# Kernel optimization log

Hardware: AMD Instinct MI355X
Metric: run time of the kernel (lower is better)

Reference implementation:

```python
import jax, jax.numpy as jnp
import numpy as np

B, L, D = 32, 1024, 1024
H = 8            # hard-coded in FourierBlock weights1 leading dim
E = D // H       # 128
M = 64           # number of retained low-frequency modes
K = 25           # moving_avg kernel (stride 1)
PAD = (K - 1) // 2


def setup_inputs() -> dict:
    key = jax.random.key(0)
    ks = jax.random.split(key, 7)
    scale = 1.0 / (D * D)
    return {
        "x":   jax.random.normal(ks[0], (B, L, D), jnp.float32),
        "Wq":  jax.random.normal(ks[1], (D, D), jnp.float32) * 0.02,
        "bq":  jax.random.normal(ks[2], (D,), jnp.float32) * 0.02,
        "w1r": jax.random.uniform(ks[3], (H, E, E, M), jnp.float32) * scale,
        "w1i": jax.random.uniform(ks[4], (H, E, E, M), jnp.float32) * scale,
        "Wo":  jax.random.normal(ks[5], (D, D), jnp.float32) * 0.02,
        "bo":  jax.random.normal(ks[6], (D,), jnp.float32) * 0.02,
    }


def _forward(x, Wq, bq, w1r, w1i, Wo, bo):
    # --- AutoCorrelationLayer query projection (k,v projections are dead code in FourierBlock) ---
    q = (x @ Wq + bq).reshape(B, L, H, E)          # [B,L,H,E]
    # --- FourierBlock ---
    xq = q.transpose(0, 2, 3, 1)                   # [B,H,E,L]
    x_ft = jnp.fft.rfft(xq, axis=-1)               # [B,H,E,F], F=L//2+1, complex64
    w = w1r + 1j * w1i                             # [H,E,E,M]
    # mode_select='low': index = [0..M-1], output slot wi == i
    out_sel = jnp.einsum("bhem,heom->bhom", x_ft[..., :M], w)   # [B,H,E,M]
    F = L // 2 + 1
    out_ft = jnp.zeros((B, H, E, F), dtype=x_ft.dtype).at[..., :M].set(out_sel)
    y = jnp.fft.irfft(out_ft, n=L, axis=-1)        # [B,H,E,L] real
    # faithful to torch: .view(B, L, -1) on contiguous (B,H,E,L) = flat C-order reshape
    out = y.reshape(B, L, H * E)
    new_x = out @ Wo + bo                          # out_projection
    x2 = x + new_x                                 # dropout is identity in eval
    # --- series_decomp (moving average k=25, replicate padding, stride 1) ---
    xp = jnp.concatenate(
        [jnp.repeat(x2[:, :1], PAD, axis=1), x2, jnp.repeat(x2[:, -1:], PAD, axis=1)],
        axis=1)                                    # [B, L+2*PAD, D]
    cs = jnp.cumsum(xp, axis=1)
    cs = jnp.concatenate([jnp.zeros_like(cs[:, :1]), cs], axis=1)
    moving_mean = (cs[:, K:] - cs[:, :-K]) / K     # [B,L,D]
    res = x2 - moving_mean
    return res


def reference(x, Wq, bq, w1r, w1i, Wo, bo):
    # module returns (x, attn) with attn=None; we return the array output
    return _forward(x, Wq, bq, w1r, w1i, Wo, bo)
```

## Files before the change

### kernel.cpp

```cpp
#include <hip/hip_runtime.h>
#include <hip/hip_bf16.h>

typedef __bf16 bf16x8 __attribute__((ext_vector_type(8)));
typedef float f32x4 __attribute__((ext_vector_type(4)));
typedef unsigned short u16;
typedef unsigned int u32;
typedef unsigned long long u64;


static __device__ __forceinline__ u16 f2b(float f) {
  u32 u = __builtin_bit_cast(u32, f);
  u32 r = (u + 0x7FFFu + ((u >> 16) & 1u)) >> 16;
  return (u16)r;
}
static __device__ __forceinline__ u32 pk2(float lo, float hi) {
  return (u32)f2b(lo) | ((u32)f2b(hi) << 16);
}
static __device__ __forceinline__ f32x4 mfma16(bf16x8 a, bf16x8 b, f32x4 c) {
  return __builtin_amdgcn_mfma_f32_16x16x32_bf16(a, b, c, 0, 0, 0);
}

__global__ __launch_bounds__(256) void k_prep(
    const float* __restrict__ Wq, const float* __restrict__ Wo,
    u16* __restrict__ FT, u16* __restrict__ FI2,
    u16* __restrict__ Wq16, u16* __restrict__ Wo16) {
  int idx = blockIdx.x * 256 + threadIdx.x;
  const float W0 = 6.283185307179586f / 1024.0f;
  if (idx < 131072) {
    int m2 = idx >> 10, l = idx & 1023;
    int m = (m2 < 64) ? m2 : (m2 - 64);
    int t = (m * l) & 1023;
    float s, c;
    __sincosf((float)t * W0, &s, &c);
    FT[idx] = f2b((m2 < 64) ? c : -s);
  } else if (idx < 262144) {
    int jj = idx - 131072;
    int j = jj >> 10, l = jj & 1023;
    int m = j >> 1;
    int t = (m * l) & 1023;
    float s, c;
    __sincosf((float)t * W0, &s, &c);
    float v;
    if ((j & 1) == 0) v = (m == 0) ? (1.0f / 1024.0f) : c * (2.0f / 1024.0f);
    else              v = (m == 0) ? 0.0f : -s * (2.0f / 1024.0f);
    FI2[jj] = f2b(v);
  } else if (idx < 262144 + 1048576) {
    int k = idx - 262144;
    Wq16[k] = f2b(Wq[k]);
  } else {
    int k = idx - 1310720;
    Wo16[k] = f2b(Wo[k]);
  }
}

__global__ __launch_bounds__(256) void k_wtrans(
    const float* __restrict__ w1r, const float* __restrict__ w1i,
    u16* __restrict__ W2r, u16* __restrict__ W2i) {
  __shared__ float T[128 * 65];
  int h = blockIdx.x >> 7, e = blockIdx.x & 127;
  int tid = threadIdx.x;
  for (int pass = 0; pass < 2; ++pass) {
    const float* src = pass ? w1i : w1r;
    u16* dst = pass ? W2i : W2r;
    {
      int m = tid & 63, og = tid >> 6;
      const float* sp = src + (((size_t)h * 128 + e) * 128) * 64 + m;
      for (int k = 0; k < 32; ++k) {
        int o = og * 32 + k;
        T[o * 65 + m] = sp[(size_t)o * 64];
      }
    }
    __syncthreads();
    {
      int o = tid & 127, mg = tid >> 7;
      for (int k = 0; k < 32; ++k) {
        int m = mg * 32 + k;
        dst[(((size_t)h * 64 + m) * 128 + e) * 128 + o] = f2b(T[o * 65 + m]);
      }
    }
    __syncthreads();
  }
}

template <int KSTEPS, bool BIAS, bool TSTORE>
static __device__ __forceinline__ void gemm128_db(
    const u16* __restrict__ A, size_t arow0, int astride,
    const u16* __restrict__ Bm, int bcol0,
    u16* __restrict__ C, size_t crow0, const float* __restrict__ bias) {
  __shared__ __align__(16) u16 Al[128 * 40];
  __shared__ __align__(16) u16 Bl[128 * 40];
  int tid = threadIdx.x, lane = tid & 63, w = tid >> 6;
  f32x4 acc[2][8];
#pragma unroll
  for (int i = 0; i < 2; i++)
#pragma unroll
    for (int j = 0; j < 8; j++) acc[i][j] = (f32x4){0.f, 0.f, 0.f, 0.f};
  int ar = tid >> 1, ahalf = tid & 1;
  int dloc = tid & 127, lg = tid >> 7;
  const u16* aptr = A + (arow0 + ar) * (size_t)astride + ahalf * 16;
  const u16* bptr = Bm + (size_t)(lg * 16) * 1024 + bcol0 + dloc;
  uint4 av0, av1;
  u16 bs[16];
  av0 = *(const uint4*)aptr;
  av1 = *(const uint4*)(aptr + 8);
#pragma unroll
  for (int jj = 0; jj < 4; ++jj) {
    const u16* bp = bptr + (size_t)(jj * 4) * 1024;
    bs[jj * 4 + 0] = bp[0]; bs[jj * 4 + 1] = bp[1024];
    bs[jj * 4 + 2] = bp[2048]; bs[jj * 4 + 3] = bp[3072];
  }
  for (int kk = 0; kk < KSTEPS; ++kk) {
    {
      uint4* dst = (uint4*)(Al + ar * 40 + ahalf * 16);
      dst[0] = av0; dst[1] = av1;
    }
#pragma unroll
    for (int jj = 0; jj < 4; ++jj) {
      int l0 = lg * 16 + jj * 4;
      *(u64*)(Bl + dloc * 40 + l0) = (u64)bs[jj * 4] | ((u64)bs[jj * 4 + 1] << 16) |
                                     ((u64)bs[jj * 4 + 2] << 32) | ((u64)bs[jj * 4 + 3] << 48);
    }
    __syncthreads();
    if (kk + 1 < KSTEPS) {
      const u16* ap = aptr + (kk + 1) * 32;
      av0 = *(const uint4*)ap;
      av1 = *(const uint4*)(ap + 8);
      const u16* bk = bptr + (size_t)((kk + 1) * 32) * 1024;
#pragma unroll
      for (int jj = 0; jj < 4; ++jj) {
        const u16* bp = bk + (size_t)(jj * 4) * 1024;
        bs[jj * 4 + 0] = bp[0]; bs[jj * 4 + 1] = bp[1024];
        bs[jj * 4 + 2] = bp[2048]; bs[jj * 4 + 3] = bp[3072];
      }
    }
    bf16x8 af[2];
#pragma unroll
    for (int mi = 0; mi < 2; mi++)
      af[mi] = *(const bf16x8*)(Al + (w * 32 + mi * 16 + (lane & 15)) * 40 + 8 * (lane >> 4));
#pragma unroll
    for (int ni = 0; ni < 8; ni++) {
      bf16x8 bf = *(const bf16x8*)(Bl + (ni * 16 + (lane & 15)) * 40 + 8 * (lane >> 4));
#pragma unroll
      for (int mi = 0; mi < 2; mi++) acc[mi][ni] = mfma16(af[mi], bf, acc[mi][ni]);
    }
    __syncthreads();
  }
  if (BIAS) {
    if (w == 0 && (lane >> 4) == 0) {
#pragma unroll
      for (int ni = 0; ni < 8; ni++)
        acc[0][ni][0] += 1024.0f * bias[bcol0 + ni * 16 + (lane & 15)];
    }
  }
  if (TSTORE) {
#pragma unroll
    for (int mi = 0; mi < 2; mi++)
#pragma unroll
      for (int ni = 0; ni < 8; ni++) {
        int row0 = w * 32 + mi * 16 + 4 * (lane >> 4);
        int col = bcol0 + ni * 16 + (lane & 15);
        u64 pk = (u64)f2b(acc[mi][ni][0]) | ((u64)f2b(acc[mi][ni][1]) << 16) |
                 ((u64)f2b(acc[mi][ni][2]) << 32) | ((u64)f2b(acc[mi][ni][3]) << 48);
        *(u64*)(C + (size_t)col * 128 + row0) = pk;
      }
  } else {
#pragma unroll
    for (int mi = 0; mi < 2; mi++)
#pragma unroll
      for (int ni = 0; ni < 8; ni++)
#pragma unroll
        for (int r = 0; r < 4; r++) {
          int row = w * 32 + mi * 16 + 4 * (lane >> 4) + r;
          int col = bcol0 + ni * 16 + (lane & 15);
          C[(crow0 + row) * (size_t)1024 + col] = f2b(acc[mi][ni][r]);
        }
  }
}

__global__ __launch_bounds__(256) void k_dft(const float* __restrict__ x,
                                             const u16* __restrict__ FT,
                                             u16* __restrict__ Z) {
  __shared__ __align__(16) u16 Al[128 * 40];
  __shared__ __align__(16) u16 Bl[128 * 40];
  int b = blockIdx.x >> 3, ct = blockIdx.x & 7;
  int tid = threadIdx.x, lane = tid & 63, w = tid >> 6;
  f32x4 acc[2][8];
#pragma unroll
  for (int i = 0; i < 2; i++)
#pragma unroll
    for (int j = 0; j < 8; j++) acc[i][j] = (f32x4){0.f, 0.f, 0.f, 0.f};
  int ar = tid >> 1, ahalf = tid & 1;
  int c = tid & 127, lg = tid >> 7;
  const u16* aptr = FT + ar * 1024 + ahalf * 16;
  const float* bbase = x + ((size_t)b * 1024) * 1024 + ct * 128 + c;
  uint4 av0, av1;
  float bx[16];
  av0 = *(const uint4*)aptr;
  av1 = *(const uint4*)(aptr + 8);
#pragma unroll
  for (int jj = 0; jj < 4; ++jj) {
    const float* bp = bbase + (size_t)(lg * 16 + jj * 4) * 1024;
    bx[jj * 4 + 0] = bp[0]; bx[jj * 4 + 1] = bp[1024];
    bx[jj * 4 + 2] = bp[2048]; bx[jj * 4 + 3] = bp[3072];
  }
  for (int kk = 0; kk < 32; ++kk) {
    {
      uint4* dst = (uint4*)(Al + ar * 40 + ahalf * 16);
      dst[0] = av0; dst[1] = av1;
    }
#pragma unroll
    for (int jj = 0; jj < 4; ++jj) {
      uint2 p = {pk2(bx[jj * 4], bx[jj * 4 + 1]), pk2(bx[jj * 4 + 2], bx[jj * 4 + 3])};
      *(uint2*)(Bl + c * 40 + lg * 16 + jj * 4) = p;
    }
    __syncthreads();
    if (kk < 31) {
      const u16* ap = aptr + (kk + 1) * 32;
      av0 = *(const uint4*)ap;
      av1 = *(const uint4*)(ap + 8);
      const float* bk = bbase + (size_t)((kk + 1) * 32) * 1024;
#pragma unroll
      for (int jj = 0; jj < 4; ++jj) {
        const float* bp = bk + (size_t)(jj * 4) * 1024;
        bx[jj * 4 + 0] = bp[0]; bx[jj * 4 + 1] = bp[1024];
        bx[jj * 4 + 2] = bp[2048]; bx[jj * 4 + 3] = bp[3072];
      }
    }
    bf16x8 af[2];
#pragma unroll
    for (int mi = 0; mi < 2; mi++)
      af[mi] = *(const bf16x8*)(Al + (w * 32 + mi * 16 + (lane & 15)) * 40 + 8 * (lane >> 4));
#pragma unroll
    for (int ni = 0; ni < 8; ni++) {
      bf16x8 bf = *(const bf16x8*)(Bl + (ni * 16 + (lane & 15)) * 40 + 8 * (lane >> 4));
#pragma unroll
      for (int mi = 0; mi < 2; mi++) acc[mi][ni] = mfma16(af[mi], bf, acc[mi][ni]);
    }
    __syncthreads();
  }
#pragma unroll
  for (int mi = 0; mi < 2; mi++)
#pragma unroll
    for (int ni = 0; ni < 8; ni++)
#pragma unroll
      for (int r = 0; r < 4; r++) {
        int row = w * 32 + mi * 16 + 4 * (lane >> 4) + r;
        int col = ct * 128 + ni * 16 + (lane & 15);
        Z[((size_t)b * 128 + row) * 1024 + col] = f2b(acc[mi][ni][r]);
      }
}

__global__ __launch_bounds__(256) void k_wqmix(const u16* __restrict__ Zm,
                                               const u16* __restrict__ Wq16,
                                               const float* __restrict__ bq,
                                               u16* __restrict__ XF) {
  int mt = blockIdx.x >> 3, nt = blockIdx.x & 7;
  gemm128_db<32, true, false>(Zm, (size_t)mt * 128, 1024, Wq16, nt * 128, XF,
                              (size_t)mt * 128, bq);
}

__global__ __launch_bounds__(256) void k_gmat(const u16* __restrict__ FI2,
                                              const u16* __restrict__ Wo16,
                                              u16* __restrict__ G2T) {
  int nt = blockIdx.x;
  gemm128_db<32, false, true>(FI2, 0, 1024, Wo16, nt * 128, G2T, 0, nullptr);
}

__global__ __launch_bounds__(256) void k_modemix(const u16* __restrict__ XF,
                                                 const u16* __restrict__ W2r,
                                                 const u16* __restrict__ W2i,
                                                 u16* __restrict__ OS2T) {
  __shared__ __align__(16) u16 Wbr[128 * 40], Wbi[128 * 40];
  int h = blockIdx.x >> 6, m = blockIdx.x & 63;
  int tid = threadIdx.x, lane = tid & 63, w = tid >> 6;
  bf16x8 xar[2][4], xai[2][4];
#pragma unroll
  for (int mi = 0; mi < 2; ++mi) {
    int bb = mi * 16 + (lane & 15);
    const u16* xr = XF + ((size_t)(bb * 128 + m)) * 1024 + h * 128 + 8 * (lane >> 4);
    const u16* xi = XF + ((size_t)(bb * 128 + 64 + m)) * 1024 + h * 128 + 8 * (lane >> 4);
#pragma unroll
    for (int kk = 0; kk < 4; ++kk) {
      xar[mi][kk] = *(const bf16x8*)(xr + kk * 32);
      xai[mi][kk] = *(const bf16x8*)(xi + kk * 32);
    }
  }
  int o = tid & 127, pr = tid >> 7;
  const u16* wsrc = (pr ? W2i : W2r) + ((size_t)(h * 64 + m) * 128) * 128 + o;
  u16 ws_[32];
#pragma unroll
  for (int e = 0; e < 32; ++e) ws_[e] = wsrc[(size_t)e * 128];
  f32x4 accR[2][2], accI[2][2];
#pragma unroll
  for (int i = 0; i < 2; i++)
#pragma unroll
    for (int j = 0; j < 2; j++) {
      accR[i][j] = (f32x4){0.f, 0.f, 0.f, 0.f};
      accI[i][j] = (f32x4){0.f, 0.f, 0.f, 0.f};
    }
  for (int kk = 0; kk < 4; ++kk) {
    {
      u16* wdst = (pr ? Wbi : Wbr) + o * 40;
#pragma unroll
      for (int jj = 0; jj < 8; ++jj)
        *(u64*)(wdst + jj * 4) = (u64)ws_[jj * 4] | ((u64)ws_[jj * 4 + 1] << 16) |
                                 ((u64)ws_[jj * 4 + 2] << 32) | ((u64)ws_[jj * 4 + 3] << 48);
    }
    __syncthreads();
    if (kk < 3) {
      const u16* wk = wsrc + (size_t)((kk + 1) * 32) * 128;
#pragma unroll
      for (int e = 0; e < 32; ++e) ws_[e] = wk[(size_t)e * 128];
    }
    bf16x8 ain[2];
#pragma unroll
    for (int mi = 0; mi < 2; mi++) {
      u32 t4[4];
      __builtin_memcpy(t4, &xai[mi][kk], 16);
#pragma unroll
      for (int q = 0; q < 4; q++) t4[q] ^= 0x80008000u;
      __builtin_memcpy(&ain[mi], t4, 16);
    }
#pragma unroll
    for (int ni = 0; ni < 2; ni++) {
      int o2 = w * 32 + ni * 16 + (lane & 15);
      bf16x8 br = *(const bf16x8*)(Wbr + o2 * 40 + 8 * (lane >> 4));
      bf16x8 bi = *(const bf16x8*)(Wbi + o2 * 40 + 8 * (lane >> 4));
#pragma unroll
      for (int mi = 0; mi < 2; mi++) {
        accR[mi][ni] = mfma16(xar[mi][kk], br, accR[mi][ni]);
        accR[mi][ni] = mfma16(ain[mi], bi, accR[mi][ni]);
        accI[mi][ni] = mfma16(xar[mi][kk], bi, accI[mi][ni]);
        accI[mi][ni] = mfma16(xai[mi][kk], br, accI[mi][ni]);
      }
    }
    __syncthreads();
  }
#pragma unroll
  for (int mi = 0; mi < 2; mi++)
#pragma unroll
    for (int ni = 0; ni < 2; ni++)
#pragma unroll
      for (int rr = 0; rr < 4; rr++) {
        int brow = mi * 16 + 4 * (lane >> 4) + rr;
        int o3 = w * 32 + ni * 16 + (lane & 15);
        size_t base = (size_t)brow * 131072 + (size_t)(h * 128 + o3) * 128;
        *(u32*)(OS2T + base + 2 * m) = pk2(accR[mi][ni][rr], accI[mi][ni][rr]);
      }
}

__global__ __launch_bounds__(256) void k_nxdecomp(const float* __restrict__ x,
                                                  const u16* __restrict__ OS2T,
                                                  const u16* __restrict__ G2T,
                                                  float* __restrict__ out) {
  __shared__ float ZT[160 * 68];
  int bid = blockIdx.x;
  int rt = bid & 7, dt = (bid >> 3) & 15, b = bid >> 7;
  int r0 = rt * 128, d0 = dt * 64;
  int tid = threadIdx.x, lane = tid & 63, w = tid >> 6;
  int wr = w >> 1, wc = w & 1;
  const u16* pA[5];
#pragma unroll
  for (int mi = 0; mi < 5; ++mi) {
    int row = wr * 80 + mi * 16 + (lane & 15);
    int gr = r0 - 16 + row;
    gr = gr < 0 ? 0 : (gr > 1023 ? 1023 : gr);
    pA[mi] = OS2T + ((size_t)b * 1024 + gr) * 128 + 8 * (lane >> 4);
  }
  const u16* pB[2];
#pragma unroll
  for (int ni = 0; ni < 2; ++ni) {
    int col = d0 + wc * 32 + ni * 16 + (lane & 15);
    pB[ni] = G2T + (size_t)col * 128 + 8 * (lane >> 4);
  }
  f32x4 acc[5][2];
#pragma unroll
  for (int i = 0; i < 5; i++)
#pragma unroll
    for (int j = 0; j < 2; j++) acc[i][j] = (f32x4){0.f, 0.f, 0.f, 0.f};
  bf16x8 aC[5], bC[2], aN[5], bN[2];
#pragma unroll
  for (int i = 0; i < 5; ++i) aC[i] = *(const bf16x8*)(pA[i]);
#pragma unroll
  for (int i = 0; i < 2; ++i) bC[i] = *(const bf16x8*)(pB[i]);
#pragma unroll
  for (int kk = 0; kk < 4; ++kk) {
    if (kk < 3) {
#pragma unroll
      for (int i = 0; i < 5; ++i) aN[i] = *(const bf16x8*)(pA[i] + (kk + 1) * 32);
#pragma unroll
      for (int i = 0; i < 2; ++i) bN[i] = *(const bf16x8*)(pB[i] + (kk + 1) * 32);
    }
#pragma unroll
    for (int mi = 0; mi < 5; ++mi)
#pragma unroll
      for (int ni = 0; ni < 2; ++ni) acc[mi][ni] = mfma16(aC[mi], bC[ni], acc[mi][ni]);
    if (kk < 3) {
#pragma unroll
      for (int i = 0; i < 5; ++i) aC[i] = aN[i];
#pragma unroll
      for (int i = 0; i < 2; ++i) bC[i] = bN[i];
    }
  }
#pragma unroll
  for (int mi = 0; mi < 5; ++mi)
#pragma unroll
    for (int r = 0; r < 4; ++r) {
      int row = wr * 80 + mi * 16 + 4 * (lane >> 4) + r;
      int gr = r0 - 16 + row;
      gr = gr < 0 ? 0 : (gr > 1023 ? 1023 : gr);
      const float* xp = x + ((size_t)b * 1024 + gr) * 1024 + d0;
#pragma unroll
      for (int ni = 0; ni < 2; ++ni) {
        int col = wc * 32 + ni * 16 + (lane & 15);
        ZT[row * 68 + col] = acc[mi][ni][r] + xp[col];
      }
    }
  __syncthreads();
  {
    int c = tid & 63, h2 = tid >> 6;
    int j0 = h2 * 32;
    float s = 0.f;
#pragma unroll
    for (int u = 0; u < 25; ++u) s += ZT[(j0 + 4 + u) * 68 + c];
    for (int j = j0; j < j0 + 32; ++j) {
      float center = ZT[(j + 16) * 68 + c];
      out[((size_t)b * 1024 + r0 + j) * 1024 + d0 + c] = center - s * (1.0f / 25.0f);
      if (j < j0 + 31) s += ZT[(j + 29) * 68 + c] - ZT[(j + 4) * 68 + c];
    }
  }
}

extern "C" void kernel_launch(void* const* d_in, const int* in_sizes, int n_in,
                              void* d_out, int out_size, void* d_ws, size_t ws_size,
                              hipStream_t stream) {
  const float* x = (const float*)d_in[0];
  const float* Wq = (const float*)d_in[1];
  const float* bq = (const float*)d_in[2];
  const float* w1r = (const float*)d_in[3];
  const float* w1i = (const float*)d_in[4];
  const float* Wo = (const float*)d_in[5];

  char* ws = (char*)d_ws;
  u16* FT = (u16*)(ws + 0x000000);
  u16* FI2 = (u16*)(ws + 0x040000);
  u16* Wq16 = (u16*)(ws + 0x080000);
  u16* Wo16 = (u16*)(ws + 0x280000);
  u16* G2T = (u16*)(ws + 0x480000);
  u16* OS2T = (u16*)(ws + 0x4C0000);

  char* ob = (char*)d_out;
  u16* W2r = (u16*)(ob + 0x0000000);
  u16* W2i = (u16*)(ob + 0x1000000);
  u16* Zm = (u16*)(ob + 0x2000000);
  u16* XF = (u16*)(ob + 0x2800000);

  k_prep<<<9216, 256, 0, stream>>>(Wq, Wo, FT, FI2, Wq16, Wo16);
  k_wtrans<<<1024, 256, 0, stream>>>(w1r, w1i, W2r, W2i);
  k_gmat<<<8, 256, 0, stream>>>(FI2, Wo16, G2T);
  k_dft<<<256, 256, 0, stream>>>(x, FT, Zm);
  k_wqmix<<<256, 256, 0, stream>>>(Zm, Wq16, bq, XF);
  k_modemix<<<512, 256, 0, stream>>>(XF, W2r, W2i, OS2T);
  k_nxdecomp<<<4096, 256, 0, stream>>>(x, OS2T, G2T, (float*)d_out);
}
```

Before: 435.9 us.

## Store GEMM tile as bf16 in LDS and add x residual during moving-average pass

The final fused out-projection plus series-decomposition kernel now keeps the GEMM result tile in shared memory as bf16 instead of fp32, which halves LDS usage. The x residual is no longer added before the LDS store; it is read from global memory inside the sliding-window pass, costing four x loads per output row where there was one. The explicit register double-buffering of MFMA operands is dropped and launch bounds request four blocks per CU, aiming for higher occupancy. Rounding the GEMM output to bf16 adds precision loss, and the extra x reads (mostly L2 hits) add memory traffic.

```diff
diff --git a/kernel.cpp b/kernel.cpp
--- a/kernel.cpp
+++ b/kernel.cpp
@@ -12,6 +12,10 @@
   u32 u = __builtin_bit_cast(u32, f);
   u32 r = (u + 0x7FFFu + ((u >> 16) & 1u)) >> 16;
   return (u16)r;
+}
+static __device__ __forceinline__ float b2f(u16 s) {
+  u32 u = ((u32)s) << 16;
+  return __builtin_bit_cast(float, u);
 }
 static __device__ __forceinline__ u32 pk2(float lo, float hi) {
   return (u32)f2b(lo) | ((u32)f2b(hi) << 16);
@@ -349,11 +353,11 @@
       }
 }
 
-__global__ __launch_bounds__(256) void k_nxdecomp(const float* __restrict__ x,
-                                                  const u16* __restrict__ OS2T,
-                                                  const u16* __restrict__ G2T,
-                                                  float* __restrict__ out) {
-  __shared__ float ZT[160 * 68];
+__global__ __launch_bounds__(256, 4) void k_nxdecomp(const float* __restrict__ x,
+                                                     const u16* __restrict__ OS2T,
+                                                     const u16* __restrict__ G2T,
+                                                     float* __restrict__ out) {
+  __shared__ u16 ZT[160 * 68];
   int bid = blockIdx.x;
   int rt = bid & 7, dt = (bid >> 3) & 15, b = bid >> 7;
   int r0 = rt * 128, d0 = dt * 64;
@@ -378,55 +382,51 @@
   for (int i = 0; i < 5; i++)
 #pragma unroll
     for (int j = 0; j < 2; j++) acc[i][j] = (f32x4){0.f, 0.f, 0.f, 0.f};
-  bf16x8 aC[5], bC[2], aN[5], bN[2];
-#pragma unroll
-  for (int i = 0; i < 5; ++i) aC[i] = *(const bf16x8*)(pA[i]);
-#pragma unroll
-  for (int i = 0; i < 2; ++i) bC[i] = *(const bf16x8*)(pB[i]);
 #pragma unroll
   for (int kk = 0; kk < 4; ++kk) {
-    if (kk < 3) {
-#pragma unroll
-      for (int i = 0; i < 5; ++i) aN[i] = *(const bf16x8*)(pA[i] + (kk + 1) * 32);
-#pragma unroll
-      for (int i = 0; i < 2; ++i) bN[i] = *(const bf16x8*)(pB[i] + (kk + 1) * 32);
-    }
+    bf16x8 aC[5], bC[2];
+#pragma unroll
+    for (int i = 0; i < 5; ++i) aC[i] = *(const bf16x8*)(pA[i] + kk * 32);
+#pragma unroll
+    for (int i = 0; i < 2; ++i) bC[i] = *(const bf16x8*)(pB[i] + kk * 32);
 #pragma unroll
     for (int mi = 0; mi < 5; ++mi)
 #pragma unroll
       for (int ni = 0; ni < 2; ++ni) acc[mi][ni] = mfma16(aC[mi], bC[ni], acc[mi][ni]);
-    if (kk < 3) {
-#pragma unroll
-      for (int i = 0; i < 5; ++i) aC[i] = aN[i];
-#pragma unroll
-      for (int i = 0; i < 2; ++i) bC[i] = bN[i];
-    }
   }
 #pragma unroll
   for (int mi = 0; mi < 5; ++mi)
 #pragma unroll
-    for (int r = 0; r < 4; ++r) {
-      int row = wr * 80 + mi * 16 + 4 * (lane >> 4) + r;
-      int gr = r0 - 16 + row;
-      gr = gr < 0 ? 0 : (gr > 1023 ? 1023 : gr);
-      const float* xp = x + ((size_t)b * 1024 + gr) * 1024 + d0;
-#pragma unroll
-      for (int ni = 0; ni < 2; ++ni) {
+    for (int ni = 0; ni < 2; ++ni)
+#pragma unroll
+      for (int r = 0; r < 4; ++r) {
+        int row = wr * 80 + mi * 16 + 4 * (lane >> 4) + r;
         int col = wc * 32 + ni * 16 + (lane & 15);
-        ZT[row * 68 + col] = acc[mi][ni][r] + xp[col];
-      }
-    }
+        ZT[row * 68 + col] = f2b(acc[mi][ni][r]);
+      }
   __syncthreads();
   {
     int c = tid & 63, h2 = tid >> 6;
     int j0 = h2 * 32;
+    const float* xc = x + (size_t)b * 1048576 + d0 + c;
     float s = 0.f;
 #pragma unroll
-    for (int u = 0; u < 25; ++u) s += ZT[(j0 + 4 + u) * 68 + c];
+    for (int u = 0; u < 25; ++u) {
+      int gr = r0 + j0 - 12 + u;
+      gr = gr < 0 ? 0 : (gr > 1023 ? 1023 : gr);
+      s += b2f(ZT[(j0 + 4 + u) * 68 + c]) + xc[(size_t)gr * 1024];
+    }
+#pragma unroll 4
     for (int j = j0; j < j0 + 32; ++j) {
-      float center = ZT[(j + 16) * 68 + c];
-      out[((size_t)b * 1024 + r0 + j) * 1024 + d0 + c] = center - s * (1.0f / 25.0f);
-      if (j < j0 + 31) s += ZT[(j + 29) * 68 + c] - ZT[(j + 4) * 68 + c];
+      int jr = r0 + j;
+      float center = b2f(ZT[(j + 16) * 68 + c]) + xc[(size_t)jr * 1024];
+      out[((size_t)b * 1024 + jr) * 1024 + d0 + c] = center - s * (1.0f / 25.0f);
+      if (j < j0 + 31) {
+        int gnew = jr + 13; gnew = gnew > 1023 ? 1023 : gnew;
+        int gold = jr - 12; gold = gold < 0 ? 0 : gold;
+        s += b2f(ZT[(j + 29) * 68 + c]) + xc[(size_t)gnew * 1024] -
+             b2f(ZT[(j + 4) * 68 + c]) - xc[(size_t)gold * 1024];
+      }
     }
   }
 }
```

New measurement: 504.4 us. 1.16x slower.
